# Kernel tuning notes

Hardware: AMD Instinct MI355X
Metric: run time of the kernel (lower is better)

Reference implementation:

```python
import jax, jax.numpy as jnp
import numpy as np

T, N, DH, E = 4, 50000, 64, 800000
BN_EPS = 1e-5


def setup_inputs() -> dict:
    key = jax.random.key(0)
    ks = jax.random.split(key, 8)
    node_data = jax.random.normal(ks[0], (T, N, DH), dtype=jnp.float32)
    edge_weight = jax.random.uniform(ks[1], (E,), dtype=jnp.float32)
    W1 = jax.random.normal(ks[2], (DH, 3 * DH), dtype=jnp.float32) * 0.05
    b1 = jax.random.normal(ks[3], (DH,), dtype=jnp.float32) * 0.05
    gamma = jnp.ones((3 * DH,), dtype=jnp.float32)
    beta = jnp.zeros((3 * DH,), dtype=jnp.float32)
    src = jax.random.randint(ks[4], (E,), 0, N)
    dst = jax.random.randint(ks[5], (E,), 0, N)
    return {"node_data": node_data, "edge_weight": edge_weight, "W1": W1,
            "b1": b1, "gamma": gamma, "beta": beta, "src": src, "dst": dst}


def reference(node_data, edge_weight, W1, b1, gamma, beta, src, dst):
    # --- sparse weighted neighbor aggregation (torch.bmm with sparse ew) ---
    # msg[t, e, :] = w_e * x[t, src_e, :]
    msg = node_data[:, src, :] * edge_weight[None, :, None]          # [T, E, dh]
    agg = jnp.zeros((T, N, DH), jnp.float32).at[:, dst, :].add(msg)  # [T, N, dh]
    # Z = torch.sparse.sum(ew, dim=2); Z[Z==0]=1 (degree normalization)
    Z = jnp.zeros((N,), jnp.float32).at[dst].add(edge_weight)
    Z = jnp.where(Z == 0, 1.0, Z)
    avg_neighbor = agg / Z[None, :, None]
    # prev_state: zeros at t=0, shifted node_data otherwise
    prev = jnp.concatenate([jnp.zeros((1, N, DH), jnp.float32), node_data[:-1]], axis=0)
    inp = jnp.concatenate([node_data, prev, avg_neighbor], axis=2).reshape(T * N, 3 * DH)
    # --- ReluFCN with batchnorm (training-mode batch stats, biased var) ---
    mu = jnp.mean(inp, axis=0)
    var = jnp.mean(jnp.square(inp - mu), axis=0)
    xhat = (inp - mu) * jax.lax.rsqrt(var + BN_EPS) * gamma + beta
    out = jax.nn.relu(xhat @ W1.T + b1)
    return out.reshape(T, N, DH)
```

## Files before the change

### kernel.cpp

```cpp
#include <hip/hip_runtime.h>

#define TT 4
#define NN 50000
#define DH 64
#define EE 800000
#define BN_EPS 1e-5f
#define NB 196
#define G1 64
#define G2 256

typedef __attribute__((ext_vector_type(8))) short short8;
typedef __attribute__((ext_vector_type(4))) float floatx4;

#define WS_DEG      0
#define WS_FLAGS    200704
#define WS_ROWSTART 201728
#define WS_PX       401920
#define WS_PX2      467456
#define WS_PA       532992
#define WS_PA2      598528
#define WS_W1EFF    664064
#define WS_B1EFF    688640
#define WS_PACKED   1048576
#define WS_XB       8388608
#define WS_AVGB     34078720
#define WS_RANK     34078720

__device__ __forceinline__ unsigned short f2b(float f) {
    unsigned int u = __float_as_uint(f);
    unsigned int r = (u + 0x7FFFu + ((u >> 16) & 1u)) >> 16;
    return (unsigned short)r;
}
__device__ __forceinline__ float b2f(unsigned short u) {
    return __uint_as_float((unsigned int)u << 16);
}

__global__ __launch_bounds__(256) void k_prep_stats(
    const float* __restrict__ x, unsigned short* __restrict__ xb,
    float* __restrict__ PX, float* __restrict__ PX2,
    int* __restrict__ deg, int* __restrict__ flags) {
    int t = blockIdx.y;
    int tid = threadIdx.x;
    int pb = t * G1 + blockIdx.x;
    int gid = pb * 256 + tid;
    if (gid < NN) deg[gid] = 0;
    else if (gid < NN + NB) flags[gid - NN] = 0;

    int g = blockIdx.x * 256 + tid;
    const floatx4* xt = (const floatx4*)(x + (size_t)t * NN * 64);
    unsigned short* xbt = xb + (size_t)t * NN * 64;
    float s[4] = {0.f, 0.f, 0.f, 0.f}, s2[4] = {0.f, 0.f, 0.f, 0.f};
    for (int v = g; v < NN * 16; v += G1 * 256) {
        floatx4 d = __builtin_nontemporal_load(&xt[v]);
        ushort4 o;
        o.x = f2b(d.x); o.y = f2b(d.y); o.z = f2b(d.z); o.w = f2b(d.w);
        *(ushort4*)(xbt + (size_t)v * 4) = o;
        s[0] += d.x; s2[0] += d.x * d.x;
        s[1] += d.y; s2[1] += d.y * d.y;
        s[2] += d.z; s2[2] += d.z * d.z;
        s[3] += d.w; s2[3] += d.w * d.w;
    }
    __shared__ float ls[256 * 4], ls2[256 * 4];
#pragma unroll
    for (int j = 0; j < 4; ++j) { ls[tid * 4 + j] = s[j]; ls2[tid * 4 + j] = s2[j]; }
    __syncthreads();
    if (tid < 64) {
        int g16 = tid >> 2, comp = tid & 3;
        float rs = 0.f, rs2 = 0.f;
#pragma unroll
        for (int k = 0; k < 16; ++k) {
            int j = g16 + 16 * k;
            rs += ls[j * 4 + comp]; rs2 += ls2[j * 4 + comp];
        }
        int slot = (t * G1 + blockIdx.x) * 64 + tid;
        PX[slot] = rs; PX2[slot] = rs2;
    }
}

__global__ void k_rank(const int* __restrict__ dst, int* __restrict__ deg,
                       int* __restrict__ rank) {
    int e = blockIdx.x * 256 + threadIdx.x;
    if (e < EE) rank[e] = atomicAdd(&deg[dst[e]], 1);
}

__global__ __launch_bounds__(256) void k_scan_lb(
    const int* __restrict__ deg, int* __restrict__ flags,
    int* __restrict__ row_start) {
    int b = blockIdx.x, tid = threadIdx.x;
    int i = b * 256 + tid;
    int v = (i < NN) ? deg[i] : 0;
    __shared__ int ls[256];
    ls[tid] = v;
    __syncthreads();
    for (int off = 1; off < 256; off <<= 1) {
        int t = (tid >= off) ? ls[tid - off] : 0;
        __syncthreads();
        ls[tid] += t;
        __syncthreads();
    }
    int incl = ls[tid];
    if (tid == 0) atomicExch(&flags[b], ls[255] + 1);
    __shared__ int pre_s;
    if (tid == 0) pre_s = 0;
    __syncthreads();
    if (tid < b) {
        int f;
        do { f = atomicAdd(&flags[tid], 0); } while (f == 0);
        atomicAdd(&pre_s, f - 1);
    }
    __syncthreads();
    int excl = pre_s + incl - v;
    if (i < NN) row_start[i] = excl;
    if (i == NN - 1) row_start[NN] = excl + v;
}

__global__ void k_fill2(const int* __restrict__ src, const int* __restrict__ dst,
                        const float* __restrict__ ew, const int* __restrict__ rank,
                        const int* __restrict__ row_start, int2* __restrict__ packed) {
    int e = blockIdx.x * 256 + threadIdx.x;
    if (e < EE) {
        int p = row_start[dst[e]] + rank[e];
        packed[p] = make_int2(src[e], __float_as_int(ew[e]));
    }
}

__global__ __launch_bounds__(256) void k_agg(
    const unsigned short* __restrict__ xb, const int2* __restrict__ packed,
    const int* __restrict__ row_start, unsigned short* __restrict__ avgb) {
    int wv = __builtin_amdgcn_readfirstlane(threadIdx.x >> 6);
    int n = blockIdx.x * 4 + wv;
    int l = threadIdx.x & 63;
    int t = l >> 4;
    int cg = (l & 15) * 4;
    const unsigned short* xt = xb + (size_t)t * NN * 64 + cg;
    int rs = row_start[n], re = row_start[n + 1];
    float a0 = 0.f, a1 = 0.f, a2 = 0.f, a3 = 0.f, wsum = 0.f;
    int e = rs;
    for (; e + 8 <= re; e += 8) {
        int2 p[8];
        ushort4 v[8];
#pragma unroll
        for (int j = 0; j < 8; ++j) p[j] = packed[e + j];
#pragma unroll
        for (int j = 0; j < 8; ++j) v[j] = *(const ushort4*)(xt + (size_t)p[j].x * 64);
#pragma unroll
        for (int j = 0; j < 8; ++j) {
            float w = __int_as_float(p[j].y);
            wsum += w;
            a0 = fmaf(w, b2f(v[j].x), a0); a1 = fmaf(w, b2f(v[j].y), a1);
            a2 = fmaf(w, b2f(v[j].z), a2); a3 = fmaf(w, b2f(v[j].w), a3);
        }
    }
    for (; e < re; ++e) {
        int2 p0 = packed[e];
        float w0 = __int_as_float(p0.y);
        ushort4 v0 = *(const ushort4*)(xt + (size_t)p0.x * 64);
        wsum += w0;
        a0 = fmaf(w0, b2f(v0.x), a0); a1 = fmaf(w0, b2f(v0.y), a1);
        a2 = fmaf(w0, b2f(v0.z), a2); a3 = fmaf(w0, b2f(v0.w), a3);
    }
    float rz = (wsum == 0.f) ? 1.f : (1.f / wsum);
    ushort4 o;
    o.x = f2b(a0 * rz); o.y = f2b(a1 * rz); o.z = f2b(a2 * rz); o.w = f2b(a3 * rz);
    *(ushort4*)(avgb + (size_t)t * NN * 64 + (size_t)n * 64 + cg) = o;
}

__global__ __launch_bounds__(256) void k_stats_avg(
    const unsigned short* __restrict__ avgb, float* __restrict__ PA,
    float* __restrict__ PA2) {
    int tid = threadIdx.x;
    int g = blockIdx.x * 256 + tid;
    const short8* av = (const short8*)avgb;
    float s[8], s2[8];
#pragma unroll
    for (int j = 0; j < 8; ++j) { s[j] = 0.f; s2[j] = 0.f; }
    for (int v = g; v < TT * NN * 8; v += G2 * 256) {
        short8 d = av[v];
#pragma unroll
        for (int j = 0; j < 8; ++j) {
            float f = b2f((unsigned short)d[j]);
            s[j] += f; s2[j] += f * f;
        }
    }
    __shared__ float ls[256 * 8], ls2[256 * 8];
#pragma unroll
    for (int j = 0; j < 8; ++j) { ls[tid * 8 + j] = s[j]; ls2[tid * 8 + j] = s2[j]; }
    __syncthreads();
    if (tid < 64) {
        int g8 = tid >> 3, comp = tid & 7;
        float rs = 0.f, rs2 = 0.f;
#pragma unroll
        for (int k = 0; k < 32; ++k) {
            int j = g8 + 8 * k;
            rs += ls[j * 8 + comp]; rs2 += ls2[j * 8 + comp];
        }
        PA[blockIdx.x * 64 + tid] = rs;
        PA2[blockIdx.x * 64 + tid] = rs2;
    }
}

__global__ void k_fold(const float* __restrict__ W1, const float* __restrict__ b1,
                       const float* __restrict__ gamma, const float* __restrict__ beta,
                       const float* __restrict__ PX, const float* __restrict__ PX2,
                       const float* __restrict__ PA, const float* __restrict__ PA2,
                       unsigned short* __restrict__ W1eff, float* __restrict__ b1eff) {
    __shared__ float gS[192], hS[192];
    int c = threadIdx.x;
    const float inv = 1.0f / (float)(TT * NN);
    if (c < 192) {
        float s = 0.f, s2 = 0.f;
        if (c < 64) {
            for (int i = 0; i < TT * G1; ++i) { s += PX[i * 64 + c]; s2 += PX2[i * 64 + c]; }
        } else if (c < 128) {
            int cc = c - 64;
            for (int i = 0; i < (TT - 1) * G1; ++i) { s += PX[i * 64 + cc]; s2 += PX2[i * 64 + cc]; }
        } else {
            int cc = c - 128;
            for (int i = 0; i < G2; ++i) { s += PA[i * 64 + cc]; s2 += PA2[i * 64 + cc]; }
        }
        float mu = s * inv, ex2 = s2 * inv;
        float var = ex2 - mu * mu;
        float g = gamma[c] / sqrtf(var + BN_EPS);
        gS[c] = g;
        hS[c] = beta[c] - mu * g;
    }
    __syncthreads();
    for (int i = threadIdx.x; i < 64 * 192; i += blockDim.x) {
        int cc = i % 192;
        W1eff[i] = f2b(W1[i] * gS[cc]);
    }
    if (threadIdx.x < 64) {
        int o = threadIdx.x;
        float acc = b1[o];
        for (int cc = 0; cc < 192; ++cc) acc += hS[cc] * W1[o * 192 + cc];
        b1eff[o] = acc;
    }
}

__global__ __launch_bounds__(256) void k_main(
    const unsigned short* __restrict__ xb, const unsigned short* __restrict__ avgb,
    const unsigned short* __restrict__ Wb, const float* __restrict__ bias,
    float* __restrict__ out) {
    int wave = threadIdx.x >> 6;
    int lane = threadIdx.x & 63;
    int r0 = blockIdx.x * 64 + wave * 16;
    int m = lane & 15;
    int q = lane >> 4;

    const unsigned short* xrow = xb   + (size_t)(r0 + m) * 64 + q * 8;
    const unsigned short* prow = xb   + (size_t)(r0 - NN + m) * 64 + q * 8;
    const unsigned short* arow = avgb + (size_t)(r0 + m) * 64 + q * 8;
    bool has_prev = (r0 >= NN);

    floatx4 acc[4];
#pragma unroll
    for (int ct = 0; ct < 4; ++ct) acc[ct] = (floatx4){0.f, 0.f, 0.f, 0.f};

    const short8 zf = (short8){0, 0, 0, 0, 0, 0, 0, 0};

#pragma unroll
    for (int kc = 0; kc < 6; ++kc) {
        short8 a;
        if (kc < 2) {
            a = *(const short8*)(xrow + kc * 32);
        } else if (kc < 4) {
            a = has_prev ? *(const short8*)(prow + (kc - 2) * 32) : zf;
        } else {
            a = *(const short8*)(arow + (kc - 4) * 32);
        }
#pragma unroll
        for (int ct = 0; ct < 4; ++ct) {
            short8 b = *(const short8*)(Wb + (size_t)(ct * 16 + m) * 192 + kc * 32 + q * 8);
            acc[ct] = __builtin_amdgcn_mfma_f32_16x16x32_bf16(a, b, acc[ct], 0, 0, 0);
        }
    }

#pragma unroll
    for (int ct = 0; ct < 4; ++ct) {
        float bv = bias[ct * 16 + m];
#pragma unroll
        for (int i = 0; i < 4; ++i) {
            int row = q * 4 + i;
            __builtin_nontemporal_store(fmaxf(acc[ct][i] + bv, 0.f),
                                        &out[(size_t)(r0 + row) * 64 + ct * 16 + m]);
        }
    }
}

extern "C" void kernel_launch(void* const* d_in, const int* in_sizes, int n_in,
                              void* d_out, int out_size, void* d_ws, size_t ws_size,
                              hipStream_t stream) {
    const float* x     = (const float*)d_in[0];
    const float* ew    = (const float*)d_in[1];
    const float* W1    = (const float*)d_in[2];
    const float* b1    = (const float*)d_in[3];
    const float* gamma = (const float*)d_in[4];
    const float* beta  = (const float*)d_in[5];
    const int*   src   = (const int*)d_in[6];
    const int*   dst   = (const int*)d_in[7];
    float* out = (float*)d_out;
    char*  ws  = (char*)d_ws;

    int*   deg      = (int*)(ws + WS_DEG);
    int*   flags    = (int*)(ws + WS_FLAGS);
    int*   row_start= (int*)(ws + WS_ROWSTART);
    float* PX       = (float*)(ws + WS_PX);
    float* PX2      = (float*)(ws + WS_PX2);
    float* PA       = (float*)(ws + WS_PA);
    float* PA2      = (float*)(ws + WS_PA2);
    unsigned short* W1eff = (unsigned short*)(ws + WS_W1EFF);
    float* b1eff    = (float*)(ws + WS_B1EFF);
    int2*  packed   = (int2*)(ws + WS_PACKED);
    unsigned short* xb   = (unsigned short*)(ws + WS_XB);
    unsigned short* avgb = (unsigned short*)(ws + WS_AVGB);
    int*   rank     = (int*)(ws + WS_RANK);

    k_prep_stats<<<dim3(G1, TT), 256, 0, stream>>>(x, xb, PX, PX2, deg, flags);

    k_rank<<<(EE + 255) / 256, 256, 0, stream>>>(dst, deg, rank);

    k_scan_lb<<<NB, 256, 0, stream>>>(deg, flags, row_start);

    k_fill2<<<(EE + 255) / 256, 256, 0, stream>>>(src, dst, ew, rank, row_start, packed);

    k_agg<<<NN / 4, 256, 0, stream>>>(xb, packed, row_start, avgb);

    k_stats_avg<<<G2, 256, 0, stream>>>(avgb, PA, PA2);

    k_fold<<<1, 192, 0, stream>>>(W1, b1, gamma, beta, PX, PX2, PA, PA2, W1eff, b1eff);

    k_main<<<(TT * NN) / 64, 256, 0, stream>>>(xb, avgb, W1eff, b1eff, out);
}
```

Before: 333.7 us.

## Interleave bf16 node features node-major across timesteps for contiguous gathers

Stores the bf16 copy of node features (and the averaged-neighbour buffer) as [N][T][64] instead of [T][N][64], so one neighbour gather reads a contiguous 512-byte row covering all four timesteps. The aggregation kernel now has each half-wave handle alternate edges with 16-byte loads and combines the halves with a cross-lane shuffle. The main GEMM kernel's addressing is changed to match. Separately, the rank kernel processes four edges per thread so several atomics are in flight at once. The intent is fewer, wider random memory transactions in the gather, at the cost of strided writes in the prep kernel and an extra shuffle reduction.

```diff
diff --git a/kernel.cpp b/kernel.cpp
--- a/kernel.cpp
+++ b/kernel.cpp
@@ -8,6 +8,7 @@
 #define NB 196
 #define G1 64
 #define G2 256
+#define RB 782
 
 typedef __attribute__((ext_vector_type(8))) short short8;
 typedef __attribute__((ext_vector_type(4))) float floatx4;
@@ -48,13 +49,13 @@
 
     int g = blockIdx.x * 256 + tid;
     const floatx4* xt = (const floatx4*)(x + (size_t)t * NN * 64);
-    unsigned short* xbt = xb + (size_t)t * NN * 64;
     float s[4] = {0.f, 0.f, 0.f, 0.f}, s2[4] = {0.f, 0.f, 0.f, 0.f};
     for (int v = g; v < NN * 16; v += G1 * 256) {
         floatx4 d = __builtin_nontemporal_load(&xt[v]);
         ushort4 o;
         o.x = f2b(d.x); o.y = f2b(d.y); o.z = f2b(d.z); o.w = f2b(d.w);
-        *(ushort4*)(xbt + (size_t)v * 4) = o;
+        int n = v >> 4, cg = (v & 15) * 4;
+        *(ushort4*)(xb + (size_t)n * 256 + t * 64 + cg) = o;
         s[0] += d.x; s2[0] += d.x * d.x;
         s[1] += d.y; s2[1] += d.y * d.y;
         s[2] += d.z; s2[2] += d.z * d.z;
@@ -77,10 +78,20 @@
     }
 }
 
-__global__ void k_rank(const int* __restrict__ dst, int* __restrict__ deg,
-                       int* __restrict__ rank) {
-    int e = blockIdx.x * 256 + threadIdx.x;
-    if (e < EE) rank[e] = atomicAdd(&deg[dst[e]], 1);
+__global__ __launch_bounds__(256) void k_rank(const int* __restrict__ dst,
+                                              int* __restrict__ deg,
+                                              int* __restrict__ rank) {
+    const int S = RB * 256;
+    int e0 = blockIdx.x * 256 + threadIdx.x;
+    int e1 = e0 + S, e2 = e0 + 2 * S, e3 = e0 + 3 * S;
+    int d0 = dst[e0], d1 = dst[e1], d2 = dst[e2];
+    int d3 = (e3 < EE) ? dst[e3] : 0;
+    int r0 = atomicAdd(&deg[d0], 1);
+    int r1 = atomicAdd(&deg[d1], 1);
+    int r2 = atomicAdd(&deg[d2], 1);
+    int r3 = (e3 < EE) ? atomicAdd(&deg[d3], 1) : 0;
+    rank[e0] = r0; rank[e1] = r1; rank[e2] = r2;
+    if (e3 < EE) rank[e3] = r3;
 }
 
 __global__ __launch_bounds__(256) void k_scan_lb(
@@ -130,39 +141,54 @@
     int wv = __builtin_amdgcn_readfirstlane(threadIdx.x >> 6);
     int n = blockIdx.x * 4 + wv;
     int l = threadIdx.x & 63;
-    int t = l >> 4;
-    int cg = (l & 15) * 4;
-    const unsigned short* xt = xb + (size_t)t * NN * 64 + cg;
+    int ep = l >> 5;
+    int li = l & 31;
+    int co = li * 8;
     int rs = row_start[n], re = row_start[n + 1];
-    float a0 = 0.f, a1 = 0.f, a2 = 0.f, a3 = 0.f, wsum = 0.f;
+    float a[8];
+#pragma unroll
+    for (int k = 0; k < 8; ++k) a[k] = 0.f;
+    float wsum = 0.f;
     int e = rs;
     for (; e + 8 <= re; e += 8) {
-        int2 p[8];
-        ushort4 v[8];
-#pragma unroll
-        for (int j = 0; j < 8; ++j) p[j] = packed[e + j];
-#pragma unroll
-        for (int j = 0; j < 8; ++j) v[j] = *(const ushort4*)(xt + (size_t)p[j].x * 64);
-#pragma unroll
-        for (int j = 0; j < 8; ++j) {
+        int2 p[4];
+        short8 v[4];
+#pragma unroll
+        for (int j = 0; j < 4; ++j) p[j] = packed[e + 2 * j + ep];
+#pragma unroll
+        for (int j = 0; j < 4; ++j)
+            v[j] = *(const short8*)(xb + (size_t)p[j].x * 256 + co);
+#pragma unroll
+        for (int j = 0; j < 4; ++j) {
             float w = __int_as_float(p[j].y);
             wsum += w;
-            a0 = fmaf(w, b2f(v[j].x), a0); a1 = fmaf(w, b2f(v[j].y), a1);
-            a2 = fmaf(w, b2f(v[j].z), a2); a3 = fmaf(w, b2f(v[j].w), a3);
-        }
-    }
-    for (; e < re; ++e) {
-        int2 p0 = packed[e];
-        float w0 = __int_as_float(p0.y);
-        ushort4 v0 = *(const ushort4*)(xt + (size_t)p0.x * 64);
-        wsum += w0;
-        a0 = fmaf(w0, b2f(v0.x), a0); a1 = fmaf(w0, b2f(v0.y), a1);
-        a2 = fmaf(w0, b2f(v0.z), a2); a3 = fmaf(w0, b2f(v0.w), a3);
-    }
+#pragma unroll
+            for (int k = 0; k < 8; ++k)
+                a[k] = fmaf(w, b2f((unsigned short)v[j][k]), a[k]);
+        }
+    }
+    for (; e < re; e += 2) {
+        int ee = e + ep;
+        if (ee < re) {
+            int2 p0 = packed[ee];
+            float w = __int_as_float(p0.y);
+            short8 v0 = *(const short8*)(xb + (size_t)p0.x * 256 + co);
+            wsum += w;
+#pragma unroll
+            for (int k = 0; k < 8; ++k)
+                a[k] = fmaf(w, b2f((unsigned short)v0[k]), a[k]);
+        }
+    }
+#pragma unroll
+    for (int k = 0; k < 8; ++k) a[k] += __shfl_xor(a[k], 32, 64);
+    wsum += __shfl_xor(wsum, 32, 64);
     float rz = (wsum == 0.f) ? 1.f : (1.f / wsum);
-    ushort4 o;
-    o.x = f2b(a0 * rz); o.y = f2b(a1 * rz); o.z = f2b(a2 * rz); o.w = f2b(a3 * rz);
-    *(ushort4*)(avgb + (size_t)t * NN * 64 + (size_t)n * 64 + cg) = o;
+    if (ep == 0) {
+        short8 o;
+#pragma unroll
+        for (int k = 0; k < 8; ++k) o[k] = (short)f2b(a[k] * rz);
+        *(short8*)(avgb + (size_t)n * 256 + co) = o;
+    }
 }
 
 __global__ __launch_bounds__(256) void k_stats_avg(
@@ -244,13 +270,14 @@
     int wave = threadIdx.x >> 6;
     int lane = threadIdx.x & 63;
     int r0 = blockIdx.x * 64 + wave * 16;
+    int t0 = r0 / NN;
+    int n0 = r0 - t0 * NN;
     int m = lane & 15;
     int q = lane >> 4;
 
-    const unsigned short* xrow = xb   + (size_t)(r0 + m) * 64 + q * 8;
-    const unsigned short* prow = xb   + (size_t)(r0 - NN + m) * 64 + q * 8;
-    const unsigned short* arow = avgb + (size_t)(r0 + m) * 64 + q * 8;
-    bool has_prev = (r0 >= NN);
+    const unsigned short* xrow = xb   + (size_t)(n0 + m) * 256 + t0 * 64 + q * 8;
+    const unsigned short* arow = avgb + (size_t)(n0 + m) * 256 + t0 * 64 + q * 8;
+    bool has_prev = (t0 > 0);
 
     floatx4 acc[4];
 #pragma unroll
@@ -264,7 +291,7 @@
         if (kc < 2) {
             a = *(const short8*)(xrow + kc * 32);
         } else if (kc < 4) {
-            a = has_prev ? *(const short8*)(prow + (kc - 2) * 32) : zf;
+            a = has_prev ? *(const short8*)(xrow - 64 + (kc - 2) * 32) : zf;
         } else {
             a = *(const short8*)(arow + (kc - 4) * 32);
         }
@@ -317,7 +344,7 @@
 
     k_prep_stats<<<dim3(G1, TT), 256, 0, stream>>>(x, xb, PX, PX2, deg, flags);
 
-    k_rank<<<(EE + 255) / 256, 256, 0, stream>>>(dst, deg, rank);
+    k_rank<<<RB, 256, 0, stream>>>(dst, deg, rank);
 
     k_scan_lb<<<NB, 256, 0, stream>>>(deg, flags, row_start);
 
```

Measured after the change: 336.3 us. Within noise of the previous version (+0.8%).
